# Kernel tuning notes

Hardware: AMD Instinct MI355X
Metric: run time of the kernel (lower is better)

Reference implementation:

```python
import jax, jax.numpy as jnp
import numpy as np

ALPHA = 0.25
GAMMA = 2.0


def _calc_iou(a, b):
    # a: [A,4] anchors (y1,x1,y2,x2); b: [M,4] boxes (x1,y1,x2,y2)
    area = (b[:, 2] - b[:, 0]) * (b[:, 3] - b[:, 1])  # [M]
    iw = jnp.minimum(a[:, 3, None], b[None, :, 2]) - jnp.maximum(a[:, 1, None], b[None, :, 0])
    ih = jnp.minimum(a[:, 2, None], b[None, :, 3]) - jnp.maximum(a[:, 0, None], b[None, :, 1])
    iw = jnp.maximum(iw, 0.0)
    ih = jnp.maximum(ih, 0.0)
    ua = ((a[:, 2] - a[:, 0]) * (a[:, 3] - a[:, 1]))[:, None] + area[None, :] - iw * ih
    ua = jnp.maximum(ua, 1e-8)
    return iw * ih / ua  # [A,M]


def _detection_loss(classification, regression, annot, anchor):
    aw = anchor[:, 3] - anchor[:, 1]
    ah = anchor[:, 2] - anchor[:, 0]
    acx = anchor[:, 1] + 0.5 * aw
    acy = anchor[:, 0] + 0.5 * ah

    valid = annot[:, 4] != -1  # [M]; setup guarantees >=1 valid per image
    p = jnp.clip(classification, 1e-4, 1.0 - 1e-4)

    iou = jnp.where(valid[None, :], _calc_iou(anchor, annot[:, :4]), -1.0)  # [A,M]
    iou_max = iou.max(axis=1)
    iou_arg = iou.argmax(axis=1)
    assigned = annot[iou_arg]  # [A,5]

    big = (assigned[:, 2] - assigned[:, 0]) * (assigned[:, 3] - assigned[:, 1]) > 100.0
    pos = jnp.where(big, iou_max >= 0.5, iou_max >= 0.15)  # [A] bool
    posf = pos.astype(p.dtype)
    num_pos = posf.sum()

    C = p.shape[1]
    targets = jax.nn.one_hot(assigned[:, 4].astype(jnp.int32), C, dtype=p.dtype) * posf[:, None]

    alpha_factor = jnp.where(targets == 1.0, ALPHA, 1.0 - ALPHA)
    focal_weight = jnp.where(targets == 1.0, 1.0 - p, p)
    bce = -(targets * jnp.log(p) + (1.0 - targets) * jnp.log(1.0 - p))
    cls_loss = (alpha_factor * focal_weight ** GAMMA * bce).sum() / jnp.maximum(num_pos, 1.0)

    gw = assigned[:, 2] - assigned[:, 0]
    gh = assigned[:, 3] - assigned[:, 1]
    gcx = assigned[:, 0] + 0.5 * gw
    gcy = assigned[:, 1] + 0.5 * gh
    gw = jnp.maximum(gw, 1.0)
    gh = jnp.maximum(gh, 1.0)
    tdx = (gcx - acx) / aw
    tdy = (gcy - acy) / ah
    tdw = jnp.log(gw / aw)
    tdh = jnp.log(gh / ah)
    tgt = jnp.stack([tdy, tdx, tdh, tdw], axis=1)  # [A,4]
    diff = jnp.abs(tgt - regression)
    rl = jnp.where(diff <= 1.0 / 9.0, 0.5 * 9.0 * diff ** 2, diff - 0.5 / 9.0)
    reg_loss = jnp.where(num_pos > 0,
                         (rl * posf[:, None]).sum() / (4.0 * jnp.maximum(num_pos, 1.0)),
                         jnp.zeros((), p.dtype))
    return cls_loss, reg_loss


def _tversky_loss(y_pred, y_true, alpha=0.7, beta=0.3, gamma=4.0 / 3.0):
    bs, C = y_pred.shape[0], y_pred.shape[1]
    yp = y_pred.reshape(bs, C, -1)
    yt = y_true.reshape(bs, C, -1)
    inter = (yp * yt).sum(axis=(0, 2))
    fp = (yp * (1.0 - yt)).sum(axis=(0, 2))
    fn = ((1.0 - yp) * yt).sum(axis=(0, 2))
    score = inter / jnp.maximum(inter + alpha * fp + beta * fn, 1e-7)
    mask = (yt.sum(axis=(0, 2)) > 0).astype(y_pred.dtype)
    loss = (1.0 - score) * mask
    return loss.mean() ** gamma


def _focal_seg_loss(logits, target, alpha=0.25, gamma=2.0):
    x = logits.reshape(-1)
    y = target.reshape(-1)
    logpt = jnp.logaddexp(0.0, x) - x * y  # BCE-with-logits, stable
    pt = jnp.exp(-logpt)
    loss = (1.0 - pt) ** gamma * logpt * (alpha * y + (1.0 - alpha) * (1.0 - y))
    return loss.mean()


def reference(classifications, regressions, anchors, annotations, segmentation, seg_annot):
    anchor = anchors[0]
    cls_l, reg_l = jax.vmap(lambda c, r, a: _detection_loss(c, r, a, anchor))(
        classifications, regressions, annotations)
    cls_loss = cls_l.mean(keepdims=True)
    reg_loss = reg_l.mean(keepdims=True) * 50.0
    seg_loss = _tversky_loss(segmentation, seg_annot) + _focal_seg_loss(segmentation, seg_annot)
    return cls_loss, reg_loss, seg_loss


def setup_inputs() -> dict:
    B, A, M, NV = 32, 46035, 64, 40
    H, W, SEGC = 384, 640, 3
    ks = jax.random.split(jax.random.key(0), 12)

    classifications = jax.random.uniform(ks[0], (B, A, 1), dtype=jnp.float32)
    regressions = jax.random.normal(ks[1], (B, A, 4), dtype=jnp.float32) * 0.1

    cx = jax.random.uniform(ks[2], (A,)) * W
    cy = jax.random.uniform(ks[3], (A,)) * H
    sw = jax.random.uniform(ks[4], (A,)) * 240.0 + 8.0
    sh = jax.random.uniform(ks[5], (A,)) * 240.0 + 8.0
    anchors = jnp.stack([cy - 0.5 * sh, cx - 0.5 * sw, cy + 0.5 * sh, cx + 0.5 * sw], axis=1)[None]

    x1 = jax.random.uniform(ks[6], (B, M)) * (W - 140.0)
    y1 = jax.random.uniform(ks[7], (B, M)) * (H - 140.0)
    bw = jax.random.uniform(ks[8], (B, M)) * 126.0 + 4.0
    bh = jax.random.uniform(ks[9], (B, M)) * 126.0 + 4.0
    boxes = jnp.stack([x1, y1, x1 + bw, y1 + bh, jnp.zeros((B, M))], axis=2)
    valid = (jnp.arange(M) < NV)[None, :, None]
    annotations = jnp.where(valid, boxes, -1.0).astype(jnp.float32)

    segmentation = jax.random.normal(ks[10], (B, SEGC, H, W), dtype=jnp.float32)
    labels = jax.random.randint(ks[11], (B, H, W), 0, SEGC)
    seg_annot = jnp.moveaxis(jax.nn.one_hot(labels, SEGC, dtype=jnp.float32), -1, 1)

    return {"classifications": classifications, "regressions": regressions,
            "anchors": anchors, "annotations": annotations,
            "segmentation": segmentation, "seg_annot": seg_annot}
```

## Files before the change

### kernel.cpp

```cpp
#include <hip/hip_runtime.h>
#include <math.h>

#define A_N 46035
#define B_N 32
#define M_N 64
#define SEGC 3
#define HW 245760
#define HW4 61440
#define NBP 30
#define SEG_BLOCKS (B_N * SEGC * NBP)
#define SEG_TOTAL 23592960
#define DET_K 2
#define ABLK 90
#define DET_BLOCKS (ABLK * B_N)
#define F4_PER_BLOCK (HW4 / NBP)

#define DET_WS (3 * B_N * ABLK)
#define SEG_WS_OFF DET_WS
#define SEG_S (B_N * NBP)

__device__ __forceinline__ double waveRed(double v) {
    for (int o = 32; o; o >>= 1) v += __shfl_down(v, o, 64);
    return v;
}

__device__ __forceinline__ void det_path(
    int blk, const float* __restrict__ cls, const float* __restrict__ reg,
    const float* __restrict__ anc, const float* __restrict__ ann,
    double* __restrict__ ws)
{
    const int b = blk / ABLK;
    const int bx = blk % ABLK;
    const int tid = threadIdx.x;
    const int a_base = bx * (256 * DET_K) + tid;

    __shared__ float4 sbox[M_N];
    __shared__ float2 sal[M_N];
    __shared__ int smv;
    if (tid < M_N) {
        const float* p = &ann[(b * M_N + tid) * 5];
        const float x1 = p[0], y1 = p[1], x2 = p[2], y2 = p[3], lb = p[4];
        sbox[tid] = make_float4(x1, y1, x2, y2);
        sal[tid] = make_float2((x2 - x1) * (y2 - y1), lb);
        unsigned long long vm = __ballot(lb != -1.0f);
        if (tid == 0) smv = (int)__popcll(vm);
    }
    __syncthreads();
    const int mv = smv;

    float ax1[DET_K], ay1[DET_K], ax2[DET_K], ay2[DET_K], aarea[DET_K];
    float binter[DET_K], bua[DET_K], pc[DET_K];
    int barg[DET_K];

    #pragma unroll
    for (int k = 0; k < DET_K; ++k) {
        const int a = a_base + k * 256;
        const int al = (a < A_N) ? a : (A_N - 1);
        const float4 av = *reinterpret_cast<const float4*>(&anc[al * 4]);
        ay1[k] = av.x; ax1[k] = av.y; ay2[k] = av.z; ax2[k] = av.w;
        aarea[k] = (av.z - av.x) * (av.w - av.y);
        binter[k] = -1.0f;
        bua[k] = 1.0f;
        barg[k] = 0;
        pc[k] = cls[b * A_N + al];
    }

    #pragma unroll 4
    for (int m = 0; m < mv; ++m) {
        const float4 bb = sbox[m];
        const float ba = sal[m].x;
        #pragma unroll
        for (int k = 0; k < DET_K; ++k) {
            const float iw = fmaxf(fminf(ax2[k], bb.z) - fmaxf(ax1[k], bb.x), 0.0f);
            const float ih = fmaxf(fminf(ay2[k], bb.w) - fmaxf(ay1[k], bb.y), 0.0f);
            const float inter = iw * ih;
            const float ua = (aarea[k] + ba) - inter;
            const bool upd = inter * bua[k] > binter[k] * ua;
            binter[k] = upd ? inter : binter[k];
            bua[k]    = upd ? ua    : bua[k];
            barg[k]   = upd ? m     : barg[k];
        }
    }

    float cls_f = 0.0f, reg_f = 0.0f;
    int pos_i = 0;

    #pragma unroll
    for (int k = 0; k < DET_K; ++k) {
        const int a = a_base + k * 256;
        if (a >= A_N) continue;
        const float4 g = sbox[barg[k]];
        const float2 al2 = sal[barg[k]];

        const bool big = al2.x > 100.0f;
        const float thr = big ? 0.5f : 0.15f;
        const bool pos = binter[k] >= thr * bua[k];
        pos_i += pos ? 1 : 0;

        float p = pc[k];
        p = fminf(fmaxf(p, 1e-4f), 1.0f - 1e-4f);
        const bool t1 = pos && ((int)al2.y == 0);
        const float af = t1 ? 0.25f : 0.75f;
        const float fw = t1 ? (1.0f - p) : p;
        const float bce = t1 ? (-__logf(p)) : (-__logf(1.0f - p));
        cls_f += af * fw * fw * bce;

        if (pos) {
            const float aw = ax2[k] - ax1[k];
            const float ah = ay2[k] - ay1[k];
            const float acx = ax1[k] + 0.5f * aw;
            const float acy = ay1[k] + 0.5f * ah;
            const float gw0 = g.z - g.x;
            const float gh0 = g.w - g.y;
            const float gcx = g.x + 0.5f * gw0;
            const float gcy = g.y + 0.5f * gh0;
            const float gw = fmaxf(gw0, 1.0f);
            const float gh = fmaxf(gh0, 1.0f);
            const float rah = __builtin_amdgcn_rcpf(ah);
            const float raw = __builtin_amdgcn_rcpf(aw);
            const float t0 = (gcy - acy) * rah;
            const float t1r = (gcx - acx) * raw;
            const float t2 = __logf(gh * rah);
            const float t3 = __logf(gw * raw);

            const float4 rv = *reinterpret_cast<const float4*>(&reg[(size_t)(b * A_N + a) * 4]);
            float d, rl, s = 0.0f;
            d = fabsf(t0 - rv.x);  rl = (d <= 1.0f/9.0f) ? 4.5f*d*d : d - 0.5f/9.0f; s += rl;
            d = fabsf(t1r - rv.y); rl = (d <= 1.0f/9.0f) ? 4.5f*d*d : d - 0.5f/9.0f; s += rl;
            d = fabsf(t2 - rv.z);  rl = (d <= 1.0f/9.0f) ? 4.5f*d*d : d - 0.5f/9.0f; s += rl;
            d = fabsf(t3 - rv.w);  rl = (d <= 1.0f/9.0f) ? 4.5f*d*d : d - 0.5f/9.0f; s += rl;
            reg_f += s;
        }
    }

    double cls_c = (double)cls_f, reg_c = (double)reg_f, pos_c = (double)pos_i;

    __shared__ double sredd[3][4];
    const int wid = threadIdx.x >> 6, lane = threadIdx.x & 63;
    cls_c = waveRed(cls_c);
    reg_c = waveRed(reg_c);
    pos_c = waveRed(pos_c);
    if (lane == 0) { sredd[0][wid] = cls_c; sredd[1][wid] = reg_c; sredd[2][wid] = pos_c; }
    __syncthreads();
    if (threadIdx.x == 0) {
        double c = 0, r = 0, pp = 0;
        for (int w = 0; w < 4; ++w) { c += sredd[0][w]; r += sredd[1][w]; pp += sredd[2][w]; }
        ws[0 * (B_N * ABLK) + b * ABLK + bx] = c;
        ws[1 * (B_N * ABLK) + b * ABLK + bx] = r;
        ws[2 * (B_N * ABLK) + b * ABLK + bx] = pp;
    }
}

__device__ __forceinline__ void seg_path(
    int sblk, const float* __restrict__ pred, const float* __restrict__ annot,
    double* __restrict__ ws)
{
    const int plane = sblk / NBP;
    const int bp = sblk % NBP;
    const int c = plane % SEGC;
    const int im = plane / SEGC;
    const long base4 = (long)plane * HW4 + (long)bp * F4_PER_BLOCK;

    const float4* __restrict__ p4 = reinterpret_cast<const float4*>(pred);
    const float4* __restrict__ t4 = reinterpret_cast<const float4*>(annot);

    float sxy = 0.0f, sx = 0.0f, syv = 0.0f, foc = 0.0f;

    for (int it = 0; it < 2; ++it) {
        float4 P[4], T[4];
        #pragma unroll
        for (int j = 0; j < 4; ++j) {
            const long idx = base4 + (long)(it * 1024 + j * 256 + threadIdx.x);
            P[j] = p4[idx];
            T[j] = t4[idx];
        }
        __builtin_amdgcn_sched_barrier(0);
        #pragma unroll
        for (int j = 0; j < 4; ++j) {
            const float px[4] = { P[j].x, P[j].y, P[j].z, P[j].w };
            const float tx[4] = { T[j].x, T[j].y, T[j].z, T[j].w };
            #pragma unroll
            for (int e = 0; e < 4; ++e) {
                const float x = px[e], y = tx[e];
                const bool sel = y > 0.5f;
                sxy = fmaf(x, y, sxy);
                sx += x;
                syv += y;
                const float s = sel ? x : -x;
                const float t = __expf(-s);
                const float u = 1.0f + t;
                const float r = __builtin_amdgcn_rcpf(u);
                const float omp = t * r;
                const float logpt = __logf(u);
                const float w = fmaf(y, -0.5f, 0.75f);
                foc = fmaf(omp * omp * logpt, w, foc);
            }
        }
    }

    double inter = (double)sxy, sxd = (double)sx, ycv = (double)syv, fo = (double)foc;

    __shared__ double sreds[4][4];
    const int wid = threadIdx.x >> 6, lane = threadIdx.x & 63;
    inter = waveRed(inter);
    sxd   = waveRed(sxd);
    ycv   = waveRed(ycv);
    fo    = waveRed(fo);
    if (lane == 0) { sreds[0][wid] = inter; sreds[1][wid] = sxd; sreds[2][wid] = ycv; sreds[3][wid] = fo; }
    __syncthreads();
    if (threadIdx.x == 0) {
        double a = 0, b2 = 0, cc = 0, dd = 0;
        for (int w = 0; w < 4; ++w) { a += sreds[0][w]; b2 += sreds[1][w]; cc += sreds[2][w]; dd += sreds[3][w]; }
        const int s = im * NBP + bp;
        double* seg_ws = ws + SEG_WS_OFF;
        seg_ws[(c * 4 + 0) * SEG_S + s] = a;
        seg_ws[(c * 4 + 1) * SEG_S + s] = b2;
        seg_ws[(c * 4 + 2) * SEG_S + s] = cc;
        seg_ws[(c * 4 + 3) * SEG_S + s] = dd;
    }
}

__global__ __launch_bounds__(256) void fused_kernel(
    const float* __restrict__ cls, const float* __restrict__ reg,
    const float* __restrict__ anc, const float* __restrict__ ann,
    const float* __restrict__ pred, const float* __restrict__ annot,
    double* __restrict__ ws)
{
    const int blk = blockIdx.x;
    if ((blk & 1) == 0) {
        det_path(blk >> 1, cls, reg, anc, ann, ws);
    } else {
        seg_path(blk >> 1, pred, annot, ws);
    }
}

__global__ __launch_bounds__(1024) void fin_kernel(
    const double* __restrict__ ws, float* __restrict__ out)
{
    __shared__ double sseg[SEGC][4];
    __shared__ double sdet[3][B_N];

    const int t = threadIdx.x;

    if (t < 768) {
        const int w = t >> 6, lane = t & 63;
        const int c = w >> 2, q = w & 3;
        const double* base = ws + SEG_WS_OFF + (c * 4 + q) * SEG_S;
        double s = 0.0;
        #pragma unroll
        for (int i = 0; i < SEG_S / 64; ++i)
            s += base[i * 64 + lane];
        s = waveRed(s);
        if (lane == 0) sseg[c][q] = s;
    } else if (t < 768 + 96) {
        const int r = t - 768;
        const int q = r >> 5, b = r & 31;
        const double* base = ws + q * (B_N * ABLK) + b * ABLK;
        double s = 0.0;
        for (int i = 0; i < ABLK; ++i) s += base[i];
        sdet[q][b] = s;
    }
    __syncthreads();

    if (t == 0) {
        double clsm = 0.0, regm = 0.0;
        for (int b = 0; b < B_N; ++b) {
            const double np_ = sdet[2][b];
            const double mnp = fmax(np_, 1.0);
            clsm += sdet[0][b] / mnp;
            regm += (np_ > 0.0) ? sdet[1][b] / (4.0 * mnp) : 0.0;
        }
        clsm /= (double)B_N;
        regm = regm / (double)B_N * 50.0;

        double tsum = 0.0;
        for (int c = 0; c < SEGC; ++c) {
            const double inter = sseg[c][0];
            const double fpv = sseg[c][1] - inter;
            const double ycnt = sseg[c][2];
            const double fnv = ycnt - inter;
            const double denom = fmax(inter + 0.7 * fpv + 0.3 * fnv, 1e-7);
            const double score = inter / denom;
            const double mask = (ycnt > 0.0) ? 1.0 : 0.0;
            tsum += (1.0 - score) * mask;
        }
        const double tv = pow(tsum / 3.0, 4.0 / 3.0);
        double focm = 0.0;
        for (int c = 0; c < SEGC; ++c) focm += sseg[c][3];
        focm /= (double)SEG_TOTAL;

        out[0] = (float)clsm;
        out[1] = (float)regm;
        out[2] = (float)(tv + focm);
    }
}

extern "C" void kernel_launch(void* const* d_in, const int* in_sizes, int n_in,
                              void* d_out, int out_size, void* d_ws, size_t ws_size,
                              hipStream_t stream) {
    const float* cls    = (const float*)d_in[0];
    const float* reg    = (const float*)d_in[1];
    const float* anc    = (const float*)d_in[2];
    const float* ann    = (const float*)d_in[3];
    const float* seg    = (const float*)d_in[4];
    const float* segann = (const float*)d_in[5];
    double* ws = (double*)d_ws;
    float* out = (float*)d_out;

    fused_kernel<<<DET_BLOCKS + SEG_BLOCKS, 256, 0, stream>>>(
        cls, reg, anc, ann, seg, segann, ws);
    fin_kernel<<<1, 1024, 0, stream>>>(ws, out);
}
```

Before: 70.68 us.

## Pack IoU argmax into monotonic integer key and rebalance detection block mapping

After: 70.15 us. Within noise of the previous version (-0.7%).

```diff
diff --git a/kernel.cpp b/kernel.cpp
--- a/kernel.cpp
+++ b/kernel.cpp
@@ -10,8 +10,8 @@
 #define NBP 30
 #define SEG_BLOCKS (B_N * SEGC * NBP)
 #define SEG_TOTAL 23592960
-#define DET_K 2
-#define ABLK 90
+#define DET_K 4
+#define ABLK 45
 #define DET_BLOCKS (ABLK * B_N)
 #define F4_PER_BLOCK (HW4 / NBP)
 
@@ -48,9 +48,8 @@
     __syncthreads();
     const int mv = smv;
 
-    float ax1[DET_K], ay1[DET_K], ax2[DET_K], ay2[DET_K], aarea[DET_K];
-    float binter[DET_K], bua[DET_K], pc[DET_K];
-    int barg[DET_K];
+    float ax1[DET_K], ay1[DET_K], ax2[DET_K], ay2[DET_K], aarea[DET_K], pc[DET_K];
+    unsigned best[DET_K];
 
     #pragma unroll
     for (int k = 0; k < DET_K; ++k) {
@@ -59,9 +58,7 @@
         const float4 av = *reinterpret_cast<const float4*>(&anc[al * 4]);
         ay1[k] = av.x; ax1[k] = av.y; ay2[k] = av.z; ax2[k] = av.w;
         aarea[k] = (av.z - av.x) * (av.w - av.y);
-        binter[k] = -1.0f;
-        bua[k] = 1.0f;
-        barg[k] = 0;
+        best[k] = 0u;
         pc[k] = cls[b * A_N + al];
     }
 
@@ -69,16 +66,16 @@
     for (int m = 0; m < mv; ++m) {
         const float4 bb = sbox[m];
         const float ba = sal[m].x;
+        const unsigned idxm = 63u - (unsigned)m;
         #pragma unroll
         for (int k = 0; k < DET_K; ++k) {
             const float iw = fmaxf(fminf(ax2[k], bb.z) - fmaxf(ax1[k], bb.x), 0.0f);
             const float ih = fmaxf(fminf(ay2[k], bb.w) - fmaxf(ay1[k], bb.y), 0.0f);
             const float inter = iw * ih;
-            const float ua = (aarea[k] + ba) - inter;
-            const bool upd = inter * bua[k] > binter[k] * ua;
-            binter[k] = upd ? inter : binter[k];
-            bua[k]    = upd ? ua    : bua[k];
-            barg[k]   = upd ? m     : barg[k];
+            const float ab = aarea[k] + ba;
+            const float key = inter * __builtin_amdgcn_rcpf(ab);
+            const unsigned kb = (__float_as_uint(key) & 0xFFFFFFC0u) | idxm;
+            best[k] = best[k] > kb ? best[k] : kb;
         }
     }
 
@@ -89,12 +86,19 @@
     for (int k = 0; k < DET_K; ++k) {
         const int a = a_base + k * 256;
         if (a >= A_N) continue;
-        const float4 g = sbox[barg[k]];
-        const float2 al2 = sal[barg[k]];
+        const int barg = 63 - (int)(best[k] & 63u);
+        const float4 g = sbox[barg];
+        const float2 al2 = sal[barg];
+
+        const float iw = fmaxf(fminf(ax2[k], g.z) - fmaxf(ax1[k], g.x), 0.0f);
+        const float ih = fmaxf(fminf(ay2[k], g.w) - fmaxf(ay1[k], g.y), 0.0f);
+        const float binter = iw * ih;
+        const float bab = aarea[k] + al2.x;
 
         const bool big = al2.x > 100.0f;
+        const float c1 = big ? 1.5f : 1.15f;
         const float thr = big ? 0.5f : 0.15f;
-        const bool pos = binter[k] >= thr * bua[k];
+        const bool pos = binter * c1 >= thr * bab;
         pos_i += pos ? 1 : 0;
 
         float p = pc[k];
@@ -227,10 +231,10 @@
     double* __restrict__ ws)
 {
     const int blk = blockIdx.x;
-    if ((blk & 1) == 0) {
-        det_path(blk >> 1, cls, reg, anc, ann, ws);
+    if (blk % 3 == 0) {
+        det_path(blk / 3, cls, reg, anc, ann, ws);
     } else {
-        seg_path(blk >> 1, pred, annot, ws);
+        seg_path(blk - 1 - blk / 3, pred, annot, ws);
     }
 }
 
```

## Split seg work into more blocks, reorder block dispatch, simplify IoU compare

Applied to the files above, without the earlier changes.

Result: faster. 63.71 us, median of 2 (-9.9%).

```diff
diff --git a/kernel.cpp b/kernel.cpp
--- a/kernel.cpp
+++ b/kernel.cpp
@@ -7,7 +7,7 @@
 #define SEGC 3
 #define HW 245760
 #define HW4 61440
-#define NBP 30
+#define NBP 60
 #define SEG_BLOCKS (B_N * SEGC * NBP)
 #define SEG_TOTAL 23592960
 #define DET_K 2
@@ -16,7 +16,6 @@
 #define F4_PER_BLOCK (HW4 / NBP)
 
 #define DET_WS (3 * B_N * ABLK)
-#define SEG_WS_OFF DET_WS
 #define SEG_S (B_N * NBP)
 
 __device__ __forceinline__ double waveRed(double v) {
@@ -48,8 +47,8 @@
     __syncthreads();
     const int mv = smv;
 
-    float ax1[DET_K], ay1[DET_K], ax2[DET_K], ay2[DET_K], aarea[DET_K];
-    float binter[DET_K], bua[DET_K], pc[DET_K];
+    float ax1[DET_K], ay1[DET_K], ax2[DET_K], ay2[DET_K], aarea[DET_K], pc[DET_K];
+    float binter[DET_K], bua[DET_K];
     int barg[DET_K];
 
     #pragma unroll
@@ -74,10 +73,10 @@
             const float iw = fmaxf(fminf(ax2[k], bb.z) - fmaxf(ax1[k], bb.x), 0.0f);
             const float ih = fmaxf(fminf(ay2[k], bb.w) - fmaxf(ay1[k], bb.y), 0.0f);
             const float inter = iw * ih;
-            const float ua = (aarea[k] + ba) - inter;
-            const bool upd = inter * bua[k] > binter[k] * ua;
+            const float ab = aarea[k] + ba;
+            const bool upd = inter * bua[k] > binter[k] * ab;
             binter[k] = upd ? inter : binter[k];
-            bua[k]    = upd ? ua    : bua[k];
+            bua[k]    = upd ? ab    : bua[k];
             barg[k]   = upd ? m     : barg[k];
         }
     }
@@ -93,8 +92,9 @@
         const float2 al2 = sal[barg[k]];
 
         const bool big = al2.x > 100.0f;
+        const float c1 = big ? 1.5f : 1.15f;
         const float thr = big ? 0.5f : 0.15f;
-        const bool pos = binter[k] >= thr * bua[k];
+        const bool pos = binter[k] * c1 >= thr * bua[k];
         pos_i += pos ? 1 : 0;
 
         float p = pc[k];
@@ -153,7 +153,7 @@
 
 __device__ __forceinline__ void seg_path(
     int sblk, const float* __restrict__ pred, const float* __restrict__ annot,
-    double* __restrict__ ws)
+    float* __restrict__ seg_ws)
 {
     const int plane = sblk / NBP;
     const int bp = sblk % NBP;
@@ -164,37 +164,35 @@
     const float4* __restrict__ p4 = reinterpret_cast<const float4*>(pred);
     const float4* __restrict__ t4 = reinterpret_cast<const float4*>(annot);
 
+    float4 P[4], T[4];
+    #pragma unroll
+    for (int j = 0; j < 4; ++j) {
+        const long idx = base4 + (long)(j * 256 + threadIdx.x);
+        P[j] = p4[idx];
+        T[j] = t4[idx];
+    }
+    __builtin_amdgcn_sched_barrier(0);
+
     float sxy = 0.0f, sx = 0.0f, syv = 0.0f, foc = 0.0f;
-
-    for (int it = 0; it < 2; ++it) {
-        float4 P[4], T[4];
+    #pragma unroll
+    for (int j = 0; j < 4; ++j) {
+        const float px[4] = { P[j].x, P[j].y, P[j].z, P[j].w };
+        const float tx[4] = { T[j].x, T[j].y, T[j].z, T[j].w };
         #pragma unroll
-        for (int j = 0; j < 4; ++j) {
-            const long idx = base4 + (long)(it * 1024 + j * 256 + threadIdx.x);
-            P[j] = p4[idx];
-            T[j] = t4[idx];
-        }
-        __builtin_amdgcn_sched_barrier(0);
-        #pragma unroll
-        for (int j = 0; j < 4; ++j) {
-            const float px[4] = { P[j].x, P[j].y, P[j].z, P[j].w };
-            const float tx[4] = { T[j].x, T[j].y, T[j].z, T[j].w };
-            #pragma unroll
-            for (int e = 0; e < 4; ++e) {
-                const float x = px[e], y = tx[e];
-                const bool sel = y > 0.5f;
-                sxy = fmaf(x, y, sxy);
-                sx += x;
-                syv += y;
-                const float s = sel ? x : -x;
-                const float t = __expf(-s);
-                const float u = 1.0f + t;
-                const float r = __builtin_amdgcn_rcpf(u);
-                const float omp = t * r;
-                const float logpt = __logf(u);
-                const float w = fmaf(y, -0.5f, 0.75f);
-                foc = fmaf(omp * omp * logpt, w, foc);
-            }
+        for (int e = 0; e < 4; ++e) {
+            const float x = px[e], y = tx[e];
+            const bool sel = y > 0.5f;
+            sxy = fmaf(x, y, sxy);
+            sx += x;
+            syv += y;
+            const float s = sel ? x : -x;
+            const float t = __expf(-s);
+            const float u = 1.0f + t;
+            const float r = __builtin_amdgcn_rcpf(u);
+            const float omp = t * r;
+            const float logpt = __logf(u);
+            const float w = fmaf(y, -0.5f, 0.75f);
+            foc = fmaf(omp * omp * logpt, w, foc);
         }
     }
 
@@ -212,11 +210,10 @@
         double a = 0, b2 = 0, cc = 0, dd = 0;
         for (int w = 0; w < 4; ++w) { a += sreds[0][w]; b2 += sreds[1][w]; cc += sreds[2][w]; dd += sreds[3][w]; }
         const int s = im * NBP + bp;
-        double* seg_ws = ws + SEG_WS_OFF;
-        seg_ws[(c * 4 + 0) * SEG_S + s] = a;
-        seg_ws[(c * 4 + 1) * SEG_S + s] = b2;
-        seg_ws[(c * 4 + 2) * SEG_S + s] = cc;
-        seg_ws[(c * 4 + 3) * SEG_S + s] = dd;
+        seg_ws[(c * 4 + 0) * SEG_S + s] = (float)a;
+        seg_ws[(c * 4 + 1) * SEG_S + s] = (float)b2;
+        seg_ws[(c * 4 + 2) * SEG_S + s] = (float)cc;
+        seg_ws[(c * 4 + 3) * SEG_S + s] = (float)dd;
     }
 }
 
@@ -227,10 +224,11 @@
     double* __restrict__ ws)
 {
     const int blk = blockIdx.x;
-    if ((blk & 1) == 0) {
-        det_path(blk >> 1, cls, reg, anc, ann, ws);
+    if (blk < DET_BLOCKS) {
+        det_path(blk, cls, reg, anc, ann, ws);
     } else {
-        seg_path(blk >> 1, pred, annot, ws);
+        seg_path(blk - DET_BLOCKS, pred, annot,
+                 reinterpret_cast<float*>(ws + DET_WS));
     }
 }
 
@@ -241,15 +239,16 @@
     __shared__ double sdet[3][B_N];
 
     const int t = threadIdx.x;
+    const float* seg_ws = reinterpret_cast<const float*>(ws + DET_WS);
 
     if (t < 768) {
         const int w = t >> 6, lane = t & 63;
         const int c = w >> 2, q = w & 3;
-        const double* base = ws + SEG_WS_OFF + (c * 4 + q) * SEG_S;
+        const float* base = seg_ws + (c * 4 + q) * SEG_S;
         double s = 0.0;
         #pragma unroll
         for (int i = 0; i < SEG_S / 64; ++i)
-            s += base[i * 64 + lane];
+            s += (double)base[i * 64 + lane];
         s = waveRed(s);
         if (lane == 0) sseg[c][q] = s;
     } else if (t < 768 + 96) {
```
